# Performance work log

Hardware: AMD Instinct MI355X
Metric: run time of the kernel (lower is better)

## Reference

```python
import jax, jax.numpy as jnp
import numpy as np

B, N, D, H, C = 4, 1024, 768, 12, 3
Dh = D // H                      # 64
HID = int(D * 4.0 * (2.0 / 3.0)) # 2048 (SwiGLU hidden)
EPS = 1e-5


def layernorm(x, g, b):
    m = jnp.mean(x, axis=-1, keepdims=True)
    v = jnp.mean(jnp.square(x - m), axis=-1, keepdims=True)
    return (x - m) * jax.lax.rsqrt(v + EPS) * g + b


def setup_inputs() -> dict:
    key = jax.random.key(0)
    ks = jax.random.split(key, 8)
    x = jax.random.normal(ks[0], (B, N, D), jnp.float32)
    coords = jax.random.uniform(ks[1], (B, N, C), jnp.float32)
    qkv_w = jax.random.normal(ks[2], (3 * D, D), jnp.float32) * 0.02
    qkv_b = jnp.zeros((3 * D,), jnp.float32)
    rel_w = jax.random.normal(ks[3], (H, C), jnp.float32) * 0.1
    ln1_g = jnp.ones((D,), jnp.float32)
    ln1_b = jnp.zeros((D,), jnp.float32)
    ln2_g = jnp.ones((D,), jnp.float32)
    ln2_b = jnp.zeros((D,), jnp.float32)
    win_w = jax.random.normal(ks[4], (2 * HID, D), jnp.float32) * 0.02
    win_b = jnp.zeros((2 * HID,), jnp.float32)
    wout_w = jax.random.normal(ks[5], (D, HID), jnp.float32) * 0.02
    wout_b = jnp.zeros((D,), jnp.float32)
    return dict(x=x, coords=coords, ln1_g=ln1_g, ln1_b=ln1_b, qkv_w=qkv_w,
                qkv_b=qkv_b, rel_w=rel_w, ln2_g=ln2_g, ln2_b=ln2_b,
                win_w=win_w, win_b=win_b, wout_w=wout_w, wout_b=wout_b)


def reference(x, coords, ln1_g, ln1_b, qkv_w, qkv_b, rel_w, ln2_g, ln2_b,
              win_w, win_b, wout_w, wout_b):
    # --- PatchAttention on norm1(x) ---
    h = layernorm(x, ln1_g, ln1_b)
    qkv = h @ qkv_w.T + qkv_b                    # (B,N,3D)
    q, k, v = jnp.split(qkv, 3, axis=-1)

    def heads(t):  # (B,N,D) -> (B,H,N,Dh)
        return t.reshape(B, N, H, Dh).transpose(0, 2, 1, 3)

    qh, kh, vh = heads(q), heads(k), heads(v)
    scale = 1.0 / np.sqrt(Dh).astype(np.float32)
    scores = jnp.einsum('bhid,bhjd->bhij', qh, kh) * scale
    # coord bias: (coords_i - coords_j) . W_h  ==  p[b,h,i] - p[b,h,j]
    p = jnp.einsum('bnc,hc->bhn', coords, rel_w)  # (B,H,N)
    scores = scores + p[:, :, :, None] - p[:, :, None, :]
    attn = jax.nn.softmax(scores, axis=-1)
    o = jnp.einsum('bhij,bhjd->bhid', attn, vh)   # (B,H,N,Dh)
    o = o.transpose(0, 2, 1, 3).reshape(B, N, D)
    x = x + o

    # --- SwiGLU FFN on norm2(x) ---
    h2 = layernorm(x, ln2_g, ln2_b)
    uv = h2 @ win_w.T + win_b                     # (B,N,2*HID)
    u, g = jnp.split(uv, 2, axis=-1)
    act = jax.nn.silu(u) * g
    return x + act @ wout_w.T + wout_b
```

## Files before the change

### kernel.cpp

```cpp
#include <hip/hip_runtime.h>
#include <math.h>

typedef unsigned short u16;
typedef __bf16 bf16x8 __attribute__((ext_vector_type(8)));
typedef __bf16 bf16x4 __attribute__((ext_vector_type(4)));
typedef u16 u16x4 __attribute__((ext_vector_type(4)));
typedef float f32x4 __attribute__((ext_vector_type(4)));

#define NTOK 1024
#define DMODEL 768
#define NHEAD 12
#define LD3 2304
#define HIDDIM 2048

__device__ __forceinline__ float b2f(u16 u) {
  unsigned int t = ((unsigned int)u) << 16;
  float f;
  __builtin_memcpy(&f, &t, 4);
  return f;
}
__device__ __forceinline__ u16 f2b(float f) {
  unsigned int t;
  __builtin_memcpy(&t, &f, 4);
  t += 0x7fffu + ((t >> 16) & 1u);
  return (u16)(t >> 16);
}

__device__ __forceinline__ void gl_lds16(const u16* g, u16* l) {
  __builtin_amdgcn_global_load_lds(
      (__attribute__((address_space(1))) const unsigned int*)g,
      (__attribute__((address_space(3))) unsigned int*)l, 16, 0, 0);
}

__global__ __launch_bounds__(256) void signal_kernel(float* __restrict__ out,
                                                     int n, float c) {
  int i = blockIdx.x * 256 + threadIdx.x;
  if (i < n) out[i] = c;
}

__global__ __launch_bounds__(256) void detect_kernel(const u16* __restrict__ x,
                                                     int* __restrict__ flag) {
  __shared__ int cnt;
  if (threadIdx.x == 0) cnt = 0;
  __syncthreads();
  int bad = 0;
  for (int i = threadIdx.x; i < 4096; i += 256) {
    u16 v = x[2 * i];
    int e = (v >> 7) & 0xFF;
    if (e >= 0xC0) bad++;
  }
  atomicAdd(&cnt, bad);
  __syncthreads();
  if (threadIdx.x == 0) *flag = (cnt >= 64) ? 1 : 0;
}

struct CanonJobs {
  const void* s[13];
  u16* d[13];
  int n[13];
};

__global__ __launch_bounds__(256) void canon_kernel(CanonJobs jobs,
                                                    const int* __restrict__ flag) {
  int j = blockIdx.y;
  int n = jobs.n[j];
  const void* s = jobs.s[j];
  u16* d = jobs.d[j];
  bool isf32 = (*flag != 0);
  for (int i = blockIdx.x * 256 + threadIdx.x; i < n; i += gridDim.x * 256) {
    d[i] = isf32 ? f2b(((const float*)s)[i]) : ((const u16*)s)[i];
  }
}

__global__ __launch_bounds__(256) void ln_bf16_kernel(
    const u16* __restrict__ x, const u16* __restrict__ g,
    const u16* __restrict__ b, u16* __restrict__ out) {
  int row = blockIdx.x;
  int tid = threadIdx.x;
  const u16* xr = x + (size_t)row * DMODEL;
  float v0 = b2f(xr[tid]), v1 = b2f(xr[tid + 256]), v2 = b2f(xr[tid + 512]);
  float s = v0 + v1 + v2;
  float q = v0 * v0 + v1 * v1 + v2 * v2;
#pragma unroll
  for (int off = 32; off; off >>= 1) {
    s += __shfl_xor(s, off, 64);
    q += __shfl_xor(q, off, 64);
  }
  __shared__ float rs[4], rq[4];
  int wv = tid >> 6;
  if ((tid & 63) == 0) { rs[wv] = s; rq[wv] = q; }
  __syncthreads();
  s = rs[0] + rs[1] + rs[2] + rs[3];
  q = rq[0] + rq[1] + rq[2] + rq[3];
  float mean = s * (1.0f / 768.0f);
  float var = q * (1.0f / 768.0f) - mean * mean;
  float inv = rsqrtf(var + 1e-5f);
  u16* outr = out + (size_t)row * DMODEL;
  outr[tid]       = f2b((v0 - mean) * inv * b2f(g[tid])       + b2f(b[tid]));
  outr[tid + 256] = f2b((v1 - mean) * inv * b2f(g[tid + 256]) + b2f(b[tid + 256]));
  outr[tid + 512] = f2b((v2 - mean) * inv * b2f(g[tid + 512]) + b2f(b[tid + 512]));
}

__global__ __launch_bounds__(256) void ln_f32_kernel(
    const float* __restrict__ x, const u16* __restrict__ g,
    const u16* __restrict__ b, u16* __restrict__ out) {
  int row = blockIdx.x;
  int tid = threadIdx.x;
  const float* xr = x + (size_t)row * DMODEL;
  float v0 = xr[tid], v1 = xr[tid + 256], v2 = xr[tid + 512];
  float s = v0 + v1 + v2;
  float q = v0 * v0 + v1 * v1 + v2 * v2;
#pragma unroll
  for (int off = 32; off; off >>= 1) {
    s += __shfl_xor(s, off, 64);
    q += __shfl_xor(q, off, 64);
  }
  __shared__ float rs[4], rq[4];
  int wv = tid >> 6;
  if ((tid & 63) == 0) { rs[wv] = s; rq[wv] = q; }
  __syncthreads();
  s = rs[0] + rs[1] + rs[2] + rs[3];
  q = rq[0] + rq[1] + rq[2] + rq[3];
  float mean = s * (1.0f / 768.0f);
  float var = q * (1.0f / 768.0f) - mean * mean;
  float inv = rsqrtf(var + 1e-5f);
  u16* outr = out + (size_t)row * DMODEL;
  outr[tid]       = f2b((v0 - mean) * inv * b2f(g[tid])       + b2f(b[tid]));
  outr[tid + 256] = f2b((v1 - mean) * inv * b2f(g[tid + 256]) + b2f(b[tid + 256]));
  outr[tid + 512] = f2b((v2 - mean) * inv * b2f(g[tid + 512]) + b2f(b[tid + 512]));
}

__device__ __forceinline__ void gemm128_mainloop(
    const u16* __restrict__ A, const u16* __restrict__ W, int K,
    int mB0, int nB0, u16* Al, u16* Bl, f32x4 (&acc)[4][4]) {
  int lane = threadIdx.x & 63;
  int wv = threadIdx.x >> 6;
  int q16 = lane & 15, quad = lane >> 4;
  int mW = (wv >> 1) * 64, nW = (wv & 1) * 64;
  int srow = lane >> 2, scol = (lane & 3) * 8;
  for (int k0 = 0; k0 < K; k0 += 32) {
#pragma unroll
    for (int c = 0; c < 2; ++c) {
      int ch = wv * 2 + c;
      int r = ch * 16 + srow;
      gl_lds16(A + (size_t)(mB0 + r) * K + k0 + scol, Al + ch * 512);
      gl_lds16(W + (size_t)(nB0 + r) * K + k0 + scol, Bl + ch * 512);
    }
    __syncthreads();
    bf16x8 af[4], bfr[4];
#pragma unroll
    for (int si = 0; si < 4; ++si)
      af[si] = *(const bf16x8*)((const __bf16*)Al + (mW + si * 16 + q16) * 32 + quad * 8);
#pragma unroll
    for (int sj = 0; sj < 4; ++sj)
      bfr[sj] = *(const bf16x8*)((const __bf16*)Bl + (nW + sj * 16 + q16) * 32 + quad * 8);
#pragma unroll
    for (int si = 0; si < 4; ++si)
#pragma unroll
      for (int sj = 0; sj < 4; ++sj)
        acc[si][sj] = __builtin_amdgcn_mfma_f32_16x16x32_bf16(af[si], bfr[sj], acc[si][sj], 0, 0, 0);
    __syncthreads();
  }
}

__global__ __launch_bounds__(256) void gemm_bt(
    const u16* __restrict__ Ap, const u16* __restrict__ Wp,
    const u16* __restrict__ bias, u16* __restrict__ Cp, int Nn, int K) {
  __shared__ __align__(16) u16 Al[128 * 32], Bl[128 * 32];
  int lane = threadIdx.x & 63;
  int wv = threadIdx.x >> 6;
  int q16 = lane & 15, quad = lane >> 4;
  int mBase = blockIdx.y * 128 + (wv >> 1) * 64;
  int nBase = blockIdx.x * 128 + (wv & 1) * 64;
  f32x4 acc[4][4] = {};
  gemm128_mainloop(Ap, Wp, K, blockIdx.y * 128, blockIdx.x * 128, Al, Bl, acc);
#pragma unroll
  for (int si = 0; si < 4; ++si)
#pragma unroll
    for (int sj = 0; sj < 4; ++sj) {
      int col = nBase + sj * 16 + q16;
      float bcol = b2f(bias[col]);
#pragma unroll
      for (int r = 0; r < 4; ++r) {
        int rowi = mBase + si * 16 + quad * 4 + r;
        Cp[(size_t)rowi * Nn + col] = f2b(acc[si][sj][r] + bcol);
      }
    }
}

__global__ __launch_bounds__(256) void gemm_out_split(
    const u16* __restrict__ Ap, const u16* __restrict__ Wp,
    const u16* __restrict__ bias, const float* __restrict__ res,
    float* __restrict__ part, float* __restrict__ out) {
  __shared__ __align__(16) u16 Al[128 * 32], Bl[64 * 32];
  int lane = threadIdx.x & 63;
  int wv = threadIdx.x >> 6;
  int q16 = lane & 15, quad = lane >> 4;
  int mB0 = blockIdx.y * 128;
  int nB0 = blockIdx.x * 64;
  int kz = blockIdx.z;
  int kbase = kz * 1024;
  int mW = (wv >> 1) * 64, nW = (wv & 1) * 32;
  int srow = lane >> 2, scol = (lane & 3) * 8;
  f32x4 acc[4][2] = {};
  for (int k0 = 0; k0 < 1024; k0 += 32) {
#pragma unroll
    for (int c = 0; c < 2; ++c) {
      int ch = wv * 2 + c;
      int r = ch * 16 + srow;
      gl_lds16(Ap + (size_t)(mB0 + r) * 2048 + kbase + k0 + scol, Al + ch * 512);
    }
    {
      int r = wv * 16 + srow;
      gl_lds16(Wp + (size_t)(nB0 + r) * 2048 + kbase + k0 + scol, Bl + wv * 512);
    }
    __syncthreads();
    bf16x8 af[4], bfr[2];
#pragma unroll
    for (int si = 0; si < 4; ++si)
      af[si] = *(const bf16x8*)((const __bf16*)Al + (mW + si * 16 + q16) * 32 + quad * 8);
#pragma unroll
    for (int sj = 0; sj < 2; ++sj)
      bfr[sj] = *(const bf16x8*)((const __bf16*)Bl + (nW + sj * 16 + q16) * 32 + quad * 8);
#pragma unroll
    for (int si = 0; si < 4; ++si)
#pragma unroll
      for (int sj = 0; sj < 2; ++sj)
        acc[si][sj] = __builtin_amdgcn_mfma_f32_16x16x32_bf16(af[si], bfr[sj], acc[si][sj], 0, 0, 0);
    __syncthreads();
  }
#pragma unroll
  for (int si = 0; si < 4; ++si)
#pragma unroll
    for (int sj = 0; sj < 2; ++sj) {
      int col = nB0 + nW + sj * 16 + q16;
#pragma unroll
      for (int r = 0; r < 4; ++r) {
        int rowi = mB0 + mW + si * 16 + quad * 4 + r;
        size_t idx = (size_t)rowi * 768 + col;
        if (kz == 0) {
          part[idx] = acc[si][sj][r];
        } else {
          out[idx] = acc[si][sj][r] + b2f(bias[col]) + res[idx];
        }
      }
    }
}

__global__ __launch_bounds__(256) void add_kernel(float* __restrict__ out,
                                                  const float* __restrict__ part) {
  int i = blockIdx.x * 256 + threadIdx.x;
  f32x4 o = ((f32x4*)out)[i];
  f32x4 p = ((const f32x4*)part)[i];
#pragma unroll
  for (int r = 0; r < 4; ++r) o[r] += p[r];
  ((f32x4*)out)[i] = o;
}

__global__ __launch_bounds__(256) void ffn_in_kernel(
    const u16* __restrict__ hp, const u16* __restrict__ Wp,
    const u16* __restrict__ bias, u16* __restrict__ actp) {
  __shared__ __align__(16) u16 Al[128 * 32], Bl[128 * 32];
  int lane = threadIdx.x & 63;
  int wv = threadIdx.x >> 6;
  int q16 = lane & 15, quad = lane >> 4;
  int mB0 = blockIdx.y * 128;
  int cB0 = blockIdx.x * 64;
  int mW = (wv >> 1) * 64;
  int cW = (wv & 1) * 32;
  int srow = lane >> 2, scol = (lane & 3) * 8;
  f32x4 au[4][2] = {}, ag[4][2] = {};
  for (int k0 = 0; k0 < DMODEL; k0 += 32) {
#pragma unroll
    for (int c = 0; c < 2; ++c) {
      int ch = wv * 2 + c;
      int r = ch * 16 + srow;
      gl_lds16(hp + (size_t)(mB0 + r) * DMODEL + k0 + scol, Al + ch * 512);
      int grow = (r < 64) ? (cB0 + r) : (HIDDIM + cB0 + r - 64);
      gl_lds16(Wp + (size_t)grow * DMODEL + k0 + scol, Bl + ch * 512);
    }
    __syncthreads();
    bf16x8 af[4], wu[2], wg[2];
#pragma unroll
    for (int si = 0; si < 4; ++si)
      af[si] = *(const bf16x8*)((const __bf16*)Al + (mW + si * 16 + q16) * 32 + quad * 8);
#pragma unroll
    for (int sj = 0; sj < 2; ++sj) {
      wu[sj] = *(const bf16x8*)((const __bf16*)Bl + (cW + sj * 16 + q16) * 32 + quad * 8);
      wg[sj] = *(const bf16x8*)((const __bf16*)Bl + (64 + cW + sj * 16 + q16) * 32 + quad * 8);
    }
#pragma unroll
    for (int si = 0; si < 4; ++si)
#pragma unroll
      for (int sj = 0; sj < 2; ++sj) {
        au[si][sj] = __builtin_amdgcn_mfma_f32_16x16x32_bf16(af[si], wu[sj], au[si][sj], 0, 0, 0);
        ag[si][sj] = __builtin_amdgcn_mfma_f32_16x16x32_bf16(af[si], wg[sj], ag[si][sj], 0, 0, 0);
      }
    __syncthreads();
  }
#pragma unroll
  for (int si = 0; si < 4; ++si)
#pragma unroll
    for (int sj = 0; sj < 2; ++sj) {
      int col = cB0 + cW + sj * 16 + q16;
      float bu = b2f(bias[col]);
      float bg = b2f(bias[HIDDIM + col]);
#pragma unroll
      for (int r = 0; r < 4; ++r) {
        int rowi = mB0 + mW + si * 16 + quad * 4 + r;
        float u = au[si][sj][r] + bu;
        float g = ag[si][sj][r] + bg;
        float s = u / (1.0f + __expf(-u));
        actp[(size_t)rowi * HIDDIM + col] = f2b(s * g);
      }
    }
}

__global__ __launch_bounds__(256) void p_kernel(
    const u16* __restrict__ coords, const u16* __restrict__ relw,
    float* __restrict__ p) {
  const float LOG2E = 1.4426950408889634f;
  int idx = blockIdx.x * 256 + threadIdx.x;
  float c0 = b2f(coords[idx * 3 + 0]);
  float c1 = b2f(coords[idx * 3 + 1]);
  float c2 = b2f(coords[idx * 3 + 2]);
  int b = idx >> 10, n = idx & 1023;
#pragma unroll
  for (int h = 0; h < NHEAD; ++h) {
    float w0 = b2f(relw[h * 3 + 0]), w1 = b2f(relw[h * 3 + 1]), w2 = b2f(relw[h * 3 + 2]);
    p[(size_t)(b * NHEAD + h) * NTOK + n] = (c0 * w0 + c1 * w1 + c2 * w2) * LOG2E;
  }
}

__global__ __launch_bounds__(256) void vt_kernel(const u16* __restrict__ qkvp,
                                                 u16* __restrict__ vtp) {
  int blk = blockIdx.x;
  int b = blk / 192;
  int rem = blk % 192;
  int h = rem >> 4;
  int nt = rem & 15;
  int wv = threadIdx.x >> 6;
  int d = threadIdx.x & 63;
  int n0 = nt * 64 + wv * 16;
  const u16* src = qkvp + ((size_t)(b * NTOK) + n0) * LD3 + 2 * DMODEL + h * 64 + d;
  u16* dst = vtp + ((size_t)((b * NHEAD + h) * 64 + d)) * NTOK + n0;
#pragma unroll
  for (int c = 0; c < 2; ++c) {
    u16 buf[8] __attribute__((aligned(16)));
#pragma unroll
    for (int i = 0; i < 8; ++i) buf[i] = src[(size_t)(c * 8 + i) * LD3];
    *(uint4*)(dst + c * 8) = *(const uint4*)buf;
  }
}

__global__ __launch_bounds__(256) void attn_kernel(
    const u16* __restrict__ qkvp, const u16* __restrict__ vtp,
    const float* __restrict__ p2, const u16* __restrict__ xp,
    float* __restrict__ x1) {
  const __bf16* qb = (const __bf16*)qkvp;
  __shared__ __align__(16) u16 Kl[2][32 * 64];
  __shared__ __align__(16) u16 Vl[2][64 * 32];
  __shared__ __align__(16) u16 Pl[4][16][40];
  int lane = threadIdx.x & 63;
  int wv = threadIdx.x >> 6;
  int blk = blockIdx.x;
  int b = blk / 192;
  int rem = blk % 192;
  int h = rem >> 4;
  int i0 = ((rem & 15) * 4 + wv) * 16;
  int q16 = lane & 15, quad = lane >> 4;

  const float scl2 = 0.125f * 1.4426950408889634f;

  const __bf16* qrow = qb + ((size_t)(b * NTOK) + i0 + q16) * LD3 + h * 64;
  bf16x8 bq0 = *(const bf16x8*)(qrow + quad * 8);
  bf16x8 bq1 = *(const bf16x8*)(qrow + 32 + quad * 8);

  const float* prow = p2 + (size_t)(b * NHEAD + h) * NTOK;

  int krw = wv * 8 + (lane >> 3);
  int ks  = (lane & 7) ^ (krw & 7);
  const u16* kg0 = qkvp + (size_t)(b * NTOK) * LD3 + DMODEL + h * 64 + ks * 8;
  int vrw = wv * 16 + (lane >> 2);
  int vs  = (lane & 3) ^ (vrw & 3);
  const u16* vg0 = vtp + ((size_t)((b * NHEAD + h) * 64 + vrw)) * NTOK + vs * 8;

  float mrun = -1e30f, lsum = 0.f;
  f32x4 accO[4] = {};

  gl_lds16(kg0 + (size_t)krw * LD3, &Kl[0][wv * 512]);
  gl_lds16(vg0, &Vl[0][wv * 512]);
  __syncthreads();

  int buf = 0;
  for (int t = 0; t < 32; ++t) {
    int j0 = t * 32;
    if (t < 31) {
      gl_lds16(kg0 + (size_t)(j0 + 32 + krw) * LD3, &Kl[buf ^ 1][wv * 512]);
      gl_lds16(vg0 + j0 + 32, &Vl[buf ^ 1][wv * 512]);
    }

    const __bf16* Kb = (const __bf16*)Kl[buf];
    int kx0 = (quad ^ (q16 & 7)) << 3;
    int kx1 = ((4 | quad) ^ (q16 & 7)) << 3;
    bf16x8 ka00 = *(const bf16x8*)(Kb + q16 * 64 + kx0);
    bf16x8 ka01 = *(const bf16x8*)(Kb + q16 * 64 + kx1);
    bf16x8 ka10 = *(const bf16x8*)(Kb + (16 + q16) * 64 + kx0);
    bf16x8 ka11 = *(const bf16x8*)(Kb + (16 + q16) * 64 + kx1);
    f32x4 st0 = {}, st1 = {};
    st0 = __builtin_amdgcn_mfma_f32_16x16x32_bf16(ka00, bq0, st0, 0, 0, 0);
    st0 = __builtin_amdgcn_mfma_f32_16x16x32_bf16(ka01, bq1, st0, 0, 0, 0);
    st1 = __builtin_amdgcn_mfma_f32_16x16x32_bf16(ka10, bq0, st1, 0, 0, 0);
    st1 = __builtin_amdgcn_mfma_f32_16x16x32_bf16(ka11, bq1, st1, 0, 0, 0);

    f32x4 pjl = *(const f32x4*)(prow + j0 + 4 * quad);
    f32x4 pjh = *(const f32x4*)(prow + j0 + 16 + 4 * quad);
    float sl[4], sh[4];
#pragma unroll
    for (int r = 0; r < 4; ++r) {
      sl[r] = st0[r] * scl2 - pjl[r];
      sh[r] = st1[r] * scl2 - pjh[r];
    }
    float lm = fmaxf(fmaxf(fmaxf(sl[0], sl[1]), fmaxf(sl[2], sl[3])),
                     fmaxf(fmaxf(sh[0], sh[1]), fmaxf(sh[2], sh[3])));
    lm = fmaxf(lm, __shfl_xor(lm, 16, 64));
    lm = fmaxf(lm, __shfl_xor(lm, 32, 64));
    float mn = fmaxf(mrun, lm);
    float alpha = exp2f(mrun - mn);
    mrun = mn;
    float pl[4], ph[4];
#pragma unroll
    for (int r = 0; r < 4; ++r) {
      pl[r] = exp2f(sl[r] - mn);
      ph[r] = exp2f(sh[r] - mn);
    }
    float ts = (pl[0] + pl[1]) + (pl[2] + pl[3]) +
               (ph[0] + ph[1]) + (ph[2] + ph[3]);
    ts += __shfl_xor(ts, 16, 64);
    ts += __shfl_xor(ts, 32, 64);
    lsum = lsum * alpha + ts;

    bf16x4 w0 = {(__bf16)pl[0], (__bf16)pl[1], (__bf16)pl[2], (__bf16)pl[3]};
    bf16x4 w1 = {(__bf16)ph[0], (__bf16)ph[1], (__bf16)ph[2], (__bf16)ph[3]};
    *(bf16x4*)(&Pl[wv][q16][4 * quad]) = w0;
    *(bf16x4*)(&Pl[wv][q16][16 + 4 * quad]) = w1;
    bf16x8 ap = *(const bf16x8*)(&Pl[wv][q16][quad * 8]);

    const __bf16* Vb = (const __bf16*)Vl[buf];
    int vx = (quad ^ (q16 & 3)) << 3;
#pragma unroll
    for (int ds = 0; ds < 4; ++ds) {
      bf16x8 av = *(const bf16x8*)(Vb + (ds * 16 + q16) * 32 + vx);
      f32x4 c = accO[ds];
#pragma unroll
      for (int r = 0; r < 4; ++r) c[r] *= alpha;
      accO[ds] = __builtin_amdgcn_mfma_f32_16x16x32_bf16(av, ap, c, 0, 0, 0);
    }

    __syncthreads();
    buf ^= 1;
  }

  float rl = 1.0f / lsum;
  size_t rowbase = ((size_t)(b * NTOK) + i0 + q16) * DMODEL + h * 64;
#pragma unroll
  for (int ds = 0; ds < 4; ++ds) {
    int d0 = ds * 16 + quad * 4;
    u16x4 xv = *(const u16x4*)(xp + rowbase + d0);
    f32x4 ov;
#pragma unroll
    for (int r = 0; r < 4; ++r) ov[r] = b2f(xv[r]) + accO[ds][r] * rl;
    *(f32x4*)(x1 + rowbase + d0) = ov;
  }
}

extern "C" void kernel_launch(void* const* d_in, const int* in_sizes, int n_in,
                              void* d_out, int out_size, void* d_ws, size_t ws_size,
                              hipStream_t stream) {
  static const int esz[13] = {3145728, 12288, 768, 768, 1769472, 2304, 36,
                              768, 768, 3145728, 4096, 1572864, 768};
  float sig = -1.f;
  if (n_in != 13) {
    sig = 6000.f + 100.f * (float)n_in;
  } else {
    for (int i = 0; i < 13; ++i)
      if (in_sizes[i] != esz[i]) { sig = 1000.f + 100.f * (float)i; break; }
  }
  if (sig < 0.f && ws_size < 57258496ULL) sig = 3000.f;
  if (sig < 0.f && out_size != 3145728) sig = 3100.f;
  if (sig >= 0.f) {
    signal_kernel<<<(out_size + 255) / 256, 256, 0, stream>>>((float*)d_out, out_size, sig);
    return;
  }

  char* ws = (char*)d_ws;
  int*  flag    = (int*)ws;
  u16*  cx      = (u16*)(ws + 256);
  u16*  cqkvw   = (u16*)(ws + 6291712);
  u16*  cwinw   = (u16*)(ws + 9830656);
  u16*  cwoutw  = (u16*)(ws + 16122112);
  u16*  ccoords = (u16*)(ws + 19267840);
  u16*  cln1g   = (u16*)(ws + 19292416);
  u16*  cln1b   = (u16*)(ws + 19293952);
  u16*  cqkvb   = (u16*)(ws + 19295488);
  u16*  crelw   = (u16*)(ws + 19300096);
  u16*  cln2g   = (u16*)(ws + 19300352);
  u16*  cln2b   = (u16*)(ws + 19301888);
  u16*  cwinb   = (u16*)(ws + 19303424);
  u16*  cwoutb  = (u16*)(ws + 19311616);
  u16*  h       = (u16*)(ws + 19313152);
  u16*  qkv     = (u16*)(ws + 25604608);
  float* pbuf   = (float*)(ws + 44478976);
  float* x1     = (float*)(ws + 44675584);
  u16*  act     = qkv;
  u16*  vt      = h;
  float* part   = (float*)(ws + 256);

  detect_kernel<<<1, 256, 0, stream>>>((const u16*)d_in[0], flag);

  CanonJobs jobs;
  u16* dsts[13] = {cx, ccoords, cln1g, cln1b, cqkvw, cqkvb, crelw,
                   cln2g, cln2b, cwinw, cwinb, cwoutw, cwoutb};
  for (int i = 0; i < 13; ++i) {
    jobs.s[i] = d_in[i];
    jobs.d[i] = dsts[i];
    jobs.n[i] = in_sizes[i];
  }
  canon_kernel<<<dim3(3072, 13), 256, 0, stream>>>(jobs, flag);

  ln_bf16_kernel<<<4096, 256, 0, stream>>>(cx, cln1g, cln1b, h);
  gemm_bt<<<dim3(18, 32), 256, 0, stream>>>(h, cqkvw, cqkvb, qkv, 2304, 768);
  p_kernel<<<16, 256, 0, stream>>>(ccoords, crelw, pbuf);
  vt_kernel<<<768, 256, 0, stream>>>(qkv, vt);
  attn_kernel<<<768, 256, 0, stream>>>(qkv, vt, pbuf, cx, x1);
  ln_f32_kernel<<<4096, 256, 0, stream>>>(x1, cln2g, cln2b, h);
  ffn_in_kernel<<<dim3(32, 32), 256, 0, stream>>>(h, cwinw, cwinb, act);
  gemm_out_split<<<dim3(12, 32, 2), 256, 0, stream>>>(act, cwoutw, cwoutb, x1,
                                                      part, (float*)d_out);
  add_kernel<<<3072, 256, 0, stream>>>((float*)d_out, part);
}
```

Baseline: 293.3 us.

## Deepen attention K/V prefetch to four LDS stages and stage bias in LDS

The attention kernel moves from double-buffered K/V tiles to a four-slot ring, keeping three tiles in flight. It waits with explicit vmcnt counters and a single barrier per iteration instead of a trailing __syncthreads. The per-head coordinate bias row is copied once into LDS rather than read from global memory every iteration. The block index is also remapped so the 48 batch-head groups vary fastest, which changes L2 locality. The cost is more LDS per block, which could reduce occupancy, and hand-written waitcnt values that must exactly match the number of outstanding loads.

```diff
diff --git a/kernel.cpp b/kernel.cpp
--- a/kernel.cpp
+++ b/kernel.cpp
@@ -358,16 +358,17 @@
     const float* __restrict__ p2, const u16* __restrict__ xp,
     float* __restrict__ x1) {
   const __bf16* qb = (const __bf16*)qkvp;
-  __shared__ __align__(16) u16 Kl[2][32 * 64];
-  __shared__ __align__(16) u16 Vl[2][64 * 32];
+  __shared__ __align__(16) u16 Kl[4][32 * 64];
+  __shared__ __align__(16) u16 Vl[4][64 * 32];
   __shared__ __align__(16) u16 Pl[4][16][40];
+  __shared__ __align__(16) float Pb[1024];
   int lane = threadIdx.x & 63;
   int wv = threadIdx.x >> 6;
-  int blk = blockIdx.x;
-  int b = blk / 192;
-  int rem = blk % 192;
-  int h = rem >> 4;
-  int i0 = ((rem & 15) * 4 + wv) * 16;
+  int hw = blockIdx.x;
+  int g = hw % 48;
+  int nt = hw / 48;
+  int b = g / 12, h = g % 12;
+  int i0 = (nt * 4 + wv) * 16;
   int q16 = lane & 15, quad = lane >> 4;
 
   const float scl2 = 0.125f * 1.4426950408889634f;
@@ -388,19 +389,28 @@
   float mrun = -1e30f, lsum = 0.f;
   f32x4 accO[4] = {};
 
-  gl_lds16(kg0 + (size_t)krw * LD3, &Kl[0][wv * 512]);
-  gl_lds16(vg0, &Vl[0][wv * 512]);
-  __syncthreads();
-
-  int buf = 0;
+  gl_lds16((const u16*)(prow + wv * 256 + lane * 4), (u16*)&Pb[wv * 256]);
+#pragma unroll
+  for (int tt = 0; tt < 3; ++tt) {
+    gl_lds16(kg0 + (size_t)(tt * 32 + krw) * LD3, &Kl[tt][wv * 512]);
+    gl_lds16(vg0 + tt * 32, &Vl[tt][wv * 512]);
+  }
+
   for (int t = 0; t < 32; ++t) {
+    if (t < 30)       asm volatile("s_waitcnt vmcnt(4)" ::: "memory");
+    else if (t == 30) asm volatile("s_waitcnt vmcnt(2)" ::: "memory");
+    else              asm volatile("s_waitcnt vmcnt(0)" ::: "memory");
+    __builtin_amdgcn_sched_barrier(0);
+    __builtin_amdgcn_s_barrier();
+    __builtin_amdgcn_sched_barrier(0);
+    if (t < 29) {
+      int j = (t + 3) * 32;
+      gl_lds16(kg0 + (size_t)(j + krw) * LD3, &Kl[(t + 3) & 3][wv * 512]);
+      gl_lds16(vg0 + j, &Vl[(t + 3) & 3][wv * 512]);
+    }
+
     int j0 = t * 32;
-    if (t < 31) {
-      gl_lds16(kg0 + (size_t)(j0 + 32 + krw) * LD3, &Kl[buf ^ 1][wv * 512]);
-      gl_lds16(vg0 + j0 + 32, &Vl[buf ^ 1][wv * 512]);
-    }
-
-    const __bf16* Kb = (const __bf16*)Kl[buf];
+    const __bf16* Kb = (const __bf16*)Kl[t & 3];
     int kx0 = (quad ^ (q16 & 7)) << 3;
     int kx1 = ((4 | quad) ^ (q16 & 7)) << 3;
     bf16x8 ka00 = *(const bf16x8*)(Kb + q16 * 64 + kx0);
@@ -413,8 +423,8 @@
     st1 = __builtin_amdgcn_mfma_f32_16x16x32_bf16(ka10, bq0, st1, 0, 0, 0);
     st1 = __builtin_amdgcn_mfma_f32_16x16x32_bf16(ka11, bq1, st1, 0, 0, 0);
 
-    f32x4 pjl = *(const f32x4*)(prow + j0 + 4 * quad);
-    f32x4 pjh = *(const f32x4*)(prow + j0 + 16 + 4 * quad);
+    f32x4 pjl = *(const f32x4*)(&Pb[j0 + 4 * quad]);
+    f32x4 pjh = *(const f32x4*)(&Pb[j0 + 16 + 4 * quad]);
     float sl[4], sh[4];
 #pragma unroll
     for (int r = 0; r < 4; ++r) {
@@ -446,7 +456,7 @@
     *(bf16x4*)(&Pl[wv][q16][16 + 4 * quad]) = w1;
     bf16x8 ap = *(const bf16x8*)(&Pl[wv][q16][quad * 8]);
 
-    const __bf16* Vb = (const __bf16*)Vl[buf];
+    const __bf16* Vb = (const __bf16*)Vl[t & 3];
     int vx = (quad ^ (q16 & 3)) << 3;
 #pragma unroll
     for (int ds = 0; ds < 4; ++ds) {
@@ -456,9 +466,6 @@
       for (int r = 0; r < 4; ++r) c[r] *= alpha;
       accO[ds] = __builtin_amdgcn_mfma_f32_16x16x32_bf16(av, ap, c, 0, 0, 0);
     }
-
-    __syncthreads();
-    buf ^= 1;
   }
 
   float rl = 1.0f / lsum;
```

Result: no change. 289.2 us (-1.4%).
